# Optimization experiments

Hardware: AMD Instinct MI355X
Metric: run time of the kernel (lower is better)

## Reference

```python
import jax, jax.numpy as jnp
import numpy as np

BATCH, L, E = 8192, 4096, 12  # E = log2(L) butterfly stages


def setup_inputs() -> dict:
    key = jax.random.key(0)
    kx, kw = jax.random.split(key)
    x = jax.random.normal(kx, (BATCH, L), dtype=jnp.float32)
    # Stacked per-stage weights: stage s has an (L, 2) coefficient table
    # (matches nn.Parameter(torch.randn(L, 2)) for each of E stages).
    W = jax.random.normal(kw, (E, L, 2), dtype=jnp.float32)
    return {"x": x, "W": W}


def _butterfly(x, W):
    # rightmost=True: apply the smallest-stride factor first (stride 1 -> L/2).
    B = x.shape[0]
    e = W.shape[0]
    y = x
    for s in range(e):
        d = 1 << s                      # pairing stride at this stage
        g = L // (2 * d)                # number of butterfly groups
        yr = y.reshape(B, g, 2, d)      # pairs (i, i ^ d) along last dim
        Wr = W[s].reshape(g, 2, d, 2)   # per-row 2x2 mix coefficients
        top, bot = yr[:, :, 0, :], yr[:, :, 1, :]
        new_top = Wr[:, 0, :, 0] * top + Wr[:, 0, :, 1] * bot
        new_bot = Wr[:, 1, :, 0] * bot + Wr[:, 1, :, 1] * top
        y = jnp.stack([new_top, new_bot], axis=2).reshape(B, L)
    return y


def reference(x, W):
    return _butterfly(x, W)
```

## Files before the change

kernel.cpp:

```cpp
#include <hip/hip_runtime.h>


constexpr int LROW = 4096;
constexpr int RPB  = 4;
constexpr int NBLK = 8192 / RPB;

__global__ __launch_bounds__(256)
__attribute__((amdgpu_waves_per_eu(4, 5)))
void butterfly12_kernel(const float* __restrict__ x,
                        const float* __restrict__ W,
                        float* __restrict__ out)
{
    __shared__ float2 lds[LROW];

    const int t  = threadIdx.x;
    const int hi = t >> 4;
    const int lo = t & 15;
    const size_t row0 = (size_t)blockIdx.x * RPB;

    float v[RPB][16];

    #pragma unroll
    for (int r = 0; r < RPB; ++r) {
        const float4* xr = reinterpret_cast<const float4*>(x + (row0 + r) * LROW);
        #pragma unroll
        for (int m = 0; m < 4; ++m) {
            const float4 q = xr[t * 4 + m];
            v[r][4*m+0] = q.x; v[r][4*m+1] = q.y;
            v[r][4*m+2] = q.z; v[r][4*m+3] = q.w;
        }
    }

    #pragma unroll
    for (int b = 0; b < 4; ++b) {
        const float* wb = W + ((size_t)b * LROW + 16 * t) * 2;
        const int dl = 1 << b;
        #pragma unroll
        for (int g = 0; g < 16; g += 2*dl)
            #pragma unroll
            for (int m = 0; m < dl; ++m) {
                const int a = g + m, c = a + dl;
                const float2 wa = *reinterpret_cast<const float2*>(wb + 2*a);
                const float2 wc = *reinterpret_cast<const float2*>(wb + 2*c);
                #pragma unroll
                for (int r = 0; r < RPB; ++r) {
                    const float va = v[r][a], vb = v[r][c];
                    v[r][a] = wa.x * va + wa.y * vb;
                    v[r][c] = wc.x * vb + wc.y * va;
                }
            }
    }

    #pragma unroll
    for (int h = 0; h < 2; ++h) {
        if (h) __syncthreads();
        #pragma unroll
        for (int i = 0; i < 16; ++i)
            lds[hi*256 + i*16 + (lo ^ i)] = make_float2(v[2*h][i], v[2*h+1][i]);
        __syncthreads();
        #pragma unroll
        for (int j = 0; j < 16; ++j) {
            const float2 q = lds[hi*256 + lo*16 + (j ^ lo)];
            v[2*h][j] = q.x; v[2*h+1][j] = q.y;
        }
    }

    #pragma unroll
    for (int b = 0; b < 4; ++b) {
        const float* wb = W + ((size_t)(4 + b) * LROW + hi*256 + lo) * 2;
        const int dl = 1 << b;
        #pragma unroll
        for (int g = 0; g < 16; g += 2*dl)
            #pragma unroll
            for (int m = 0; m < dl; ++m) {
                const int a = g + m, c = a + dl;
                const float2 wa = *reinterpret_cast<const float2*>(wb + 32*a);
                const float2 wc = *reinterpret_cast<const float2*>(wb + 32*c);
                #pragma unroll
                for (int r = 0; r < RPB; ++r) {
                    const float va = v[r][a], vb = v[r][c];
                    v[r][a] = wa.x * va + wa.y * vb;
                    v[r][c] = wc.x * vb + wc.y * va;
                }
            }
    }

    #pragma unroll
    for (int h = 0; h < 2; ++h) {
        if (h) __syncthreads();
        #pragma unroll
        for (int j = 0; j < 16; ++j)
            lds[hi*256 + lo*16 + (j ^ lo)] = make_float2(v[2*h][j], v[2*h+1][j]);
        __syncthreads();
        const int slot = lo*16 + (hi ^ lo);
        #pragma unroll
        for (int k = 0; k < 16; ++k) {
            const float2 q = lds[k*256 + slot];
            v[2*h][k] = q.x; v[2*h+1][k] = q.y;
        }
    }

    #pragma unroll
    for (int b = 0; b < 4; ++b) {
        const float* wb = W + ((size_t)(8 + b) * LROW + t) * 2;
        const int dl = 1 << b;
        #pragma unroll
        for (int g = 0; g < 16; g += 2*dl)
            #pragma unroll
            for (int m = 0; m < dl; ++m) {
                const int a = g + m, c = a + dl;
                const float2 wa = *reinterpret_cast<const float2*>(wb + 512*a);
                const float2 wc = *reinterpret_cast<const float2*>(wb + 512*c);
                #pragma unroll
                for (int r = 0; r < RPB; ++r) {
                    const float va = v[r][a], vb = v[r][c];
                    v[r][a] = wa.x * va + wa.y * vb;
                    v[r][c] = wc.x * vb + wc.y * va;
                }
            }
    }

    #pragma unroll
    for (int r = 0; r < RPB; ++r) {
        float* orow = out + (row0 + r) * LROW;
        #pragma unroll
        for (int k = 0; k < 16; ++k)
            orow[k*256 + t] = v[r][k];
    }
}

extern "C" void kernel_launch(void* const* d_in, const int* in_sizes, int n_in,
                              void* d_out, int out_size, void* d_ws, size_t ws_size,
                              hipStream_t stream) {
    const float* x = (const float*)d_in[0];
    const float* W = (const float*)d_in[1];
    float* out = (float*)d_out;

    butterfly12_kernel<<<NBLK, 256, 0, stream>>>(x, W, out);
}
```

Baseline: 321.9 us.

## Split butterfly into four 3-stage phases with wave-local LDS exchanges

Restructures the kernel from 256 threads with 16 elements each into 512 threads with 8 elements each. The 12 stages become four radix-8 phases. The first two transposes stay inside a 64-thread wave, so they need only an lgkmcnt wait instead of block barriers, and an XOR swizzle avoids LDS bank conflicts. Only the final cross-wave transpose uses __syncthreads. This lowers per-thread register pressure and the number of barriers, but adds one more LDS round trip and relies on wave-synchronous execution for correctness.

```diff
diff --git a/kernel.cpp b/kernel.cpp
--- a/kernel.cpp
+++ b/kernel.cpp
@@ -5,8 +5,14 @@
 constexpr int RPB  = 4;
 constexpr int NBLK = 8192 / RPB;
 
-__global__ __launch_bounds__(256)
-__attribute__((amdgpu_waves_per_eu(4, 5)))
+__device__ __forceinline__ int slotf(int P3, int P2, int P1, int P0) {
+    const int b012 = (P0 ^ P1 ^ P2) & 7;
+    const int b3   = (P1 ^ (P2 >> 1)) & 1;
+    const int U    = (P3 << 5) | (P2 << 2) | (P1 >> 1);
+    return (U << 4) | (b3 << 3) | b012;
+}
+
+__global__ __launch_bounds__(512)
 void butterfly12_kernel(const float* __restrict__ x,
                         const float* __restrict__ W,
                         float* __restrict__ out)
@@ -14,29 +20,40 @@
     __shared__ float2 lds[LROW];
 
     const int t  = threadIdx.x;
-    const int hi = t >> 4;
-    const int lo = t & 15;
+    const int t6 = t >> 6;
+    const int t3 = (t >> 3) & 7;
+    const int t0 = t & 7;
     const size_t row0 = (size_t)blockIdx.x * RPB;
 
-    float v[RPB][16];
+    float v[RPB][8];
 
     #pragma unroll
     for (int r = 0; r < RPB; ++r) {
-        const float4* xr = reinterpret_cast<const float4*>(x + (row0 + r) * LROW);
+        const float4* xr = reinterpret_cast<const float4*>(x + (row0 + r) * LROW + 8 * t);
+        const float4 qa = xr[0], qb = xr[1];
+        v[r][0]=qa.x; v[r][1]=qa.y; v[r][2]=qa.z; v[r][3]=qa.w;
+        v[r][4]=qb.x; v[r][5]=qb.y; v[r][6]=qb.z; v[r][7]=qb.w;
+    }
+
+    {
+        const float* w0 = W + ((size_t)0 * LROW + 8 * t) * 2;
         #pragma unroll
-        for (int m = 0; m < 4; ++m) {
-            const float4 q = xr[t * 4 + m];
-            v[r][4*m+0] = q.x; v[r][4*m+1] = q.y;
-            v[r][4*m+2] = q.z; v[r][4*m+3] = q.w;
+        for (int g = 0; g < 8; g += 2) {
+            const float4 q = *reinterpret_cast<const float4*>(w0 + 2 * g);
+            #pragma unroll
+            for (int r = 0; r < RPB; ++r) {
+                const float va = v[r][g], vb = v[r][g+1];
+                v[r][g]   = q.x * va + q.y * vb;
+                v[r][g+1] = q.z * vb + q.w * va;
+            }
         }
     }
-
     #pragma unroll
-    for (int b = 0; b < 4; ++b) {
-        const float* wb = W + ((size_t)b * LROW + 16 * t) * 2;
+    for (int b = 1; b < 3; ++b) {
+        const float* wb = W + ((size_t)b * LROW + 8 * t) * 2;
         const int dl = 1 << b;
         #pragma unroll
-        for (int g = 0; g < 16; g += 2*dl)
+        for (int g = 0; g < 8; g += 2*dl)
             #pragma unroll
             for (int m = 0; m < dl; ++m) {
                 const int a = g + m, c = a + dl;
@@ -53,29 +70,29 @@
 
     #pragma unroll
     for (int h = 0; h < 2; ++h) {
-        if (h) __syncthreads();
+        asm volatile("" ::: "memory");
         #pragma unroll
-        for (int i = 0; i < 16; ++i)
-            lds[hi*256 + i*16 + (lo ^ i)] = make_float2(v[2*h][i], v[2*h+1][i]);
-        __syncthreads();
+        for (int i = 0; i < 8; ++i)
+            lds[slotf(t6, t3, t0, i)] = make_float2(v[2*h][i], v[2*h+1][i]);
+        asm volatile("s_waitcnt lgkmcnt(0)" ::: "memory");
         #pragma unroll
-        for (int j = 0; j < 16; ++j) {
-            const float2 q = lds[hi*256 + lo*16 + (j ^ lo)];
+        for (int j = 0; j < 8; ++j) {
+            const float2 q = lds[slotf(t6, t3, j, t0)];
             v[2*h][j] = q.x; v[2*h+1][j] = q.y;
         }
     }
 
     #pragma unroll
-    for (int b = 0; b < 4; ++b) {
-        const float* wb = W + ((size_t)(4 + b) * LROW + hi*256 + lo) * 2;
+    for (int b = 0; b < 3; ++b) {
+        const float* wb = W + ((size_t)(3 + b) * LROW + t6*512 + t3*64 + t0) * 2;
         const int dl = 1 << b;
         #pragma unroll
-        for (int g = 0; g < 16; g += 2*dl)
+        for (int g = 0; g < 8; g += 2*dl)
             #pragma unroll
             for (int m = 0; m < dl; ++m) {
                 const int a = g + m, c = a + dl;
-                const float2 wa = *reinterpret_cast<const float2*>(wb + 32*a);
-                const float2 wc = *reinterpret_cast<const float2*>(wb + 32*c);
+                const float2 wa = *reinterpret_cast<const float2*>(wb + 16*a);
+                const float2 wc = *reinterpret_cast<const float2*>(wb + 16*c);
                 #pragma unroll
                 for (int r = 0; r < RPB; ++r) {
                     const float va = v[r][a], vb = v[r][c];
@@ -87,30 +104,71 @@
 
     #pragma unroll
     for (int h = 0; h < 2; ++h) {
-        if (h) __syncthreads();
+        asm volatile("" ::: "memory");
         #pragma unroll
-        for (int j = 0; j < 16; ++j)
-            lds[hi*256 + lo*16 + (j ^ lo)] = make_float2(v[2*h][j], v[2*h+1][j]);
-        __syncthreads();
-        const int slot = lo*16 + (hi ^ lo);
+        for (int j = 0; j < 8; ++j)
+            lds[slotf(t6, t3, j, t0)] = make_float2(v[2*h][j], v[2*h+1][j]);
+        asm volatile("s_waitcnt lgkmcnt(0)" ::: "memory");
         #pragma unroll
-        for (int k = 0; k < 16; ++k) {
-            const float2 q = lds[k*256 + slot];
+        for (int k = 0; k < 8; ++k) {
+            const float2 q = lds[slotf(t6, k, t3, t0)];
             v[2*h][k] = q.x; v[2*h+1][k] = q.y;
         }
     }
 
     #pragma unroll
-    for (int b = 0; b < 4; ++b) {
-        const float* wb = W + ((size_t)(8 + b) * LROW + t) * 2;
+    for (int b = 0; b < 3; ++b) {
+        const float* wb = W + ((size_t)(6 + b) * LROW + t6*512 + t3*8 + t0) * 2;
         const int dl = 1 << b;
         #pragma unroll
-        for (int g = 0; g < 16; g += 2*dl)
+        for (int g = 0; g < 8; g += 2*dl)
             #pragma unroll
             for (int m = 0; m < dl; ++m) {
                 const int a = g + m, c = a + dl;
-                const float2 wa = *reinterpret_cast<const float2*>(wb + 512*a);
-                const float2 wc = *reinterpret_cast<const float2*>(wb + 512*c);
+                const float2 wa = *reinterpret_cast<const float2*>(wb + 128*a);
+                const float2 wc = *reinterpret_cast<const float2*>(wb + 128*c);
+                #pragma unroll
+                for (int r = 0; r < RPB; ++r) {
+                    const float va = v[r][a], vb = v[r][c];
+                    v[r][a] = wa.x * va + wa.y * vb;
+                    v[r][c] = wc.x * vb + wc.y * va;
+                }
+            }
+    }
+
+    {
+        #pragma unroll
+        for (int k = 0; k < 8; ++k)
+            lds[slotf(t6, k, t3, t0)] = make_float2(v[0][k], v[1][k]);
+        __syncthreads();
+        #pragma unroll
+        for (int m = 0; m < 8; ++m) {
+            const float2 q = lds[slotf(m, t6, t3, t0)];
+            v[0][m] = q.x; v[1][m] = q.y;
+        }
+        __syncthreads();
+        #pragma unroll
+        for (int k = 0; k < 8; ++k)
+            lds[slotf(t6, k, t3, t0)] = make_float2(v[2][k], v[3][k]);
+        __syncthreads();
+        #pragma unroll
+        for (int m = 0; m < 8; ++m) {
+            const float2 q = lds[slotf(m, t6, t3, t0)];
+            v[2][m] = q.x; v[3][m] = q.y;
+        }
+    }
+
+    #pragma unroll
+    for (int b = 0; b < 3; ++b) {
+        const float* wb = W + ((size_t)(9 + b) * LROW + t) * 2;
+        const int dl = 1 << b;
+        #pragma unroll
+        for (int g = 0; g < 8; g += 2*dl)
+            #pragma unroll
+            for (int m = 0; m < dl; ++m) {
+                const int a = g + m, c = a + dl;
+                const float2 wa = *reinterpret_cast<const float2*>(wb + 1024*a);
+                const float2 wc = *reinterpret_cast<const float2*>(wb + 1024*c);
                 #pragma unroll
                 for (int r = 0; r < RPB; ++r) {
                     const float va = v[r][a], vb = v[r][c];
@@ -124,8 +182,8 @@
     for (int r = 0; r < RPB; ++r) {
         float* orow = out + (row0 + r) * LROW;
         #pragma unroll
-        for (int k = 0; k < 16; ++k)
-            orow[k*256 + t] = v[r][k];
+        for (int m = 0; m < 8; ++m)
+            orow[m*512 + t] = v[r][m];
     }
 }
 
@@ -136,5 +194,5 @@
     const float* W = (const float*)d_in[1];
     float* out = (float*)d_out;
 
-    butterfly12_kernel<<<NBLK, 256, 0, stream>>>(x, W, out);
+    butterfly12_kernel<<<NBLK, 512, 0, stream>>>(x, W, out);
 }
```

Result: faster. 258.4 us (-19.7%).
